# Kernel optimization log

Measured on AMD Instinct MI355X. Metric: run time of the kernel, lower is better.

The kernel has to match this reference:

```python
import jax, jax.numpy as jnp
import numpy as np

BN_EPS = 1e-5

def mish(x):
    return x * jnp.tanh(jax.nn.softplus(x))

def setup_inputs() -> dict:
    key = jax.random.key(0)
    k1, k2, k3 = jax.random.split(key, 3)
    B, C, D, N = 16, 512, 512, 2048
    x = jax.random.normal(k1, (B, C, N), dtype=jnp.float32)
    W = jax.random.normal(k2, (D, C), dtype=jnp.float32) * (1.0 / np.sqrt(C))
    gamma = jnp.ones((D,), dtype=jnp.float32)
    bn_beta = jnp.zeros((D,), dtype=jnp.float32)
    beta = jax.random.normal(k3, (1,), dtype=jnp.float32) * 0.1
    return {"x": x, "W": W, "gamma": gamma, "bn_beta": bn_beta, "beta": beta}

def reference(x, W, gamma, bn_beta, beta):
    # 1x1 conv: [B,C,N] -> [B,D,N]
    q = jnp.einsum('dc,bcn->bdn', W, x)
    # BatchNorm1d (training-mode batch stats, biased variance) over (B, N) per channel
    mean = jnp.mean(q, axis=(0, 2), keepdims=True)
    var = jnp.mean(jnp.square(q - mean), axis=(0, 2), keepdims=True)
    q = (q - mean) * jax.lax.rsqrt(var + BN_EPS)
    q = q * gamma[None, :, None] + bn_beta[None, :, None]
    h = mish(q)                                   # proj_key  [B,D,N]; proj_query = h^T [B,N,D]
    energy = jnp.einsum('bdn,bdm->bnm', h, h)     # bmm(Q, Q^T) -> [B,N,N]
    attn = jax.nn.softmax(energy, axis=-1)
    out_x = jnp.einsum('bdm,bnm->bdn', h, attn)   # bmm(proj_key, attn^T)
    return beta[0] * out_x + h
```

## Files before the change

### kernel.cpp

```cpp
#include <hip/hip_runtime.h>
#include <cstdint>
#include <cstddef>

#define B_DIM 16
#define C_DIM 512
#define D_DIM 512
#define N_DIM 2048
#define NSLOTS 512

typedef _Float16 half8  __attribute__((ext_vector_type(8)));
typedef _Float16 half4v __attribute__((ext_vector_type(4)));
typedef float    floatx4 __attribute__((ext_vector_type(4)));

__device__ __forceinline__ void gload_lds16(const _Float16* g, _Float16* l)
{
    __builtin_amdgcn_global_load_lds((const __attribute__((address_space(1))) void*)g,
                                     (__attribute__((address_space(3))) void*)l,
                                     16, 0, 0);
}

template<int EPI, int TRI, typename OutT>
__global__ __launch_bounds__(256, 4)
void gemm_nt(const _Float16* __restrict__ A, size_t strideA,
             const _Float16* __restrict__ Bm, size_t strideB,
             OutT* __restrict__ Cm, size_t strideC,
             int M, int Ncols, int K,
             const float* __restrict__ beta_ptr,
             const _Float16* __restrict__ Hm, size_t strideH,
             float* __restrict__ st_s, float* __restrict__ st_ss)
{
    constexpr int BK  = 64;
    constexpr int TP  = 136;
    constexpr int SMEM_HALFS = TRI ? (128 * TP) : (128 * 2 * BK);
    __shared__ _Float16 smem[SMEM_HALFS];
    _Float16* sA = smem;
    _Float16* sB = smem + 128 * BK;

    const int gx = gridDim.x, gy = gridDim.y;
    const int nwg = gx * gy * gridDim.z;
    int flat = blockIdx.x + gx * (blockIdx.y + gy * blockIdx.z);
    const int q8 = nwg >> 3;
    flat = (flat & 7) * q8 + (flat >> 3);

    int bx, by, bz;
    if (TRI) {
        int tri = flat % gx;
        bz = flat / gx;
        const int nt = Ncols >> 7;
        int r = 0;
        while (tri >= nt - r) { tri -= nt - r; ++r; }
        bx = r; by = r + tri;
    } else {
        bx = flat % gx;
        by = (flat / gx) % gy;
        bz = flat / (gx * gy);
    }

    const _Float16* Ab = A  + (size_t)bz * strideA;
    const _Float16* Bb = Bm + (size_t)bz * strideB;

    const int m0 = bx * 128;
    const int n0 = by * 128;

    const int tid  = threadIdx.x;
    const int lane = tid & 63;
    const int wv   = tid >> 6;
    const int wr   = (tid >> 7) & 1;
    const int wc   = (tid >> 6) & 1;
    const int fr   = lane & 15;
    const int hi   = lane >> 4;

    const int srow = tid >> 3;
    const int sk   = ((tid & 7) ^ (srow & 7)) * 8;

    const _Float16* gA0 = Ab + (size_t)(m0 + srow) * K + sk;
    const _Float16* gB0 = Bb + (size_t)(n0 + srow) * K + sk;
    _Float16* lA = &sA[(wv * 8) * BK];
    _Float16* lB = &sB[(wv * 8) * BK];

    const int ch0 = ((0 * 4 + hi) ^ (fr & 7)) * 8;
    const int ch1 = ((1 * 4 + hi) ^ (fr & 7)) * 8;
    const _Float16* fA = &sA[(wr * 64 + fr) * BK];
    const _Float16* fB = &sB[(wc * 64 + fr) * BK];

    floatx4 acc[4][4] = {};

    for (int k0 = 0; k0 < K; k0 += BK) {
        __syncthreads();
        #pragma unroll
        for (int p = 0; p < 4; ++p) {
            gload_lds16(gA0 + (size_t)(p * 32) * K + k0, lA + p * 32 * BK);
            gload_lds16(gB0 + (size_t)(p * 32) * K + k0, lB + p * 32 * BK);
        }
        __syncthreads();
        #pragma unroll
        for (int sub = 0; sub < 2; ++sub) {
            const int ch = (sub == 0) ? ch0 : ch1;
            half8 af[4], bf[4];
            #pragma unroll
            for (int i = 0; i < 4; ++i) af[i] = *(const half8*)(fA + i * 16 * BK + ch);
            #pragma unroll
            for (int j = 0; j < 4; ++j) bf[j] = *(const half8*)(fB + j * 16 * BK + ch);
            #pragma unroll
            for (int i = 0; i < 4; ++i)
                #pragma unroll
                for (int j = 0; j < 4; ++j)
                    acc[i][j] = __builtin_amdgcn_mfma_f32_16x16x32_f16(af[i], bf[j], acc[i][j], 0, 0, 0);
        }
    }

    float beta = 0.0f;
    const _Float16* Hb = nullptr;
    if (EPI == 1) { beta = beta_ptr[0]; Hb = Hm + (size_t)bz * strideH; }
    OutT* Cb = Cm + (size_t)bz * strideC;

    const bool mirror = TRI && (bx != by);
    if (mirror) __syncthreads();

    #pragma unroll
    for (int i = 0; i < 4; ++i) {
        const int rowb = m0 + wr * 64 + i * 16 + (hi << 2);
        #pragma unroll
        for (int j = 0; j < 4; ++j) {
            const int col = n0 + wc * 64 + j * 16 + fr;
            half4v mv;
            #pragma unroll
            for (int r = 0; r < 4; ++r) {
                size_t idx = (size_t)(rowb + r) * Ncols + col;
                float v = acc[i][j][r];
                if (EPI == 1) v = beta * v + (float)Hb[idx];
                Cb[idx] = (OutT)v;
                if (TRI) mv[r] = (_Float16)v;
            }
            if (mirror) {
                const int cl = wc * 64 + j * 16 + fr;
                const int rl = wr * 64 + i * 16 + (hi << 2);
                *(half4v*)(smem + cl * TP + rl) = mv;
            }
        }
    }

    if (mirror) {
        __syncthreads();
        #pragma unroll
        for (int k = 0; k < 8; ++k) {
            const int fl = tid + 256 * k;
            const int rr = fl >> 4;
            const int cc = (fl & 15) * 8;
            half8 v = *(const half8*)(smem + rr * TP + cc);
            *(half8*)((_Float16*)(void*)Cb + (size_t)(n0 + rr) * Ncols + m0 + cc) = v;
        }
    }

    if (EPI == 2) {
        const int p = ((bz * gy + by) << 1) + wc;
        #pragma unroll
        for (int i = 0; i < 4; ++i) {
            #pragma unroll
            for (int r = 0; r < 4; ++r) {
                float s = 0.f, ss2 = 0.f;
                #pragma unroll
                for (int j = 0; j < 4; ++j) {
                    float v = acc[i][j][r];
                    s += v; ss2 += v * v;
                }
                #pragma unroll
                for (int o = 1; o < 16; o <<= 1) {
                    s   += __shfl_xor(s,   o, 64);
                    ss2 += __shfl_xor(ss2, o, 64);
                }
                if (fr == 0) {
                    const int d = m0 + wr * 64 + i * 16 + (hi << 2) + r;
                    const size_t slot = (size_t)d * NSLOTS + p;
                    st_s[slot]  = s;
                    st_ss[slot] = ss2;
                }
            }
        }
    }
}

__global__ void transpose_convert_x(const float* __restrict__ x, _Float16* __restrict__ xT,
                                    const float* __restrict__ W, _Float16* __restrict__ Wh)
{
    const int bz = blockIdx.z;
    const int tx = threadIdx.x, ty = threadIdx.y;
    if (bz == B_DIM) {
        const int bid = blockIdx.x + blockIdx.y * gridDim.x;
        const int idx = bid * 256 + ty * 32 + tx;
        if (idx < D_DIM * C_DIM) Wh[idx] = (_Float16)W[idx];
        return;
    }
    __shared__ float tile[32][33];
    const int n0 = blockIdx.x * 32;
    const int c0 = blockIdx.y * 32;
    const float* xb = x + (size_t)bz * C_DIM * N_DIM;
    #pragma unroll
    for (int j = 0; j < 4; ++j)
        tile[ty + j * 8][tx] = xb[(size_t)(c0 + ty + j * 8) * N_DIM + n0 + tx];
    __syncthreads();
    _Float16* xtb = xT + (size_t)bz * N_DIM * C_DIM;
    #pragma unroll
    for (int j = 0; j < 4; ++j)
        xtb[(size_t)(n0 + ty + j * 8) * C_DIM + c0 + tx] = (_Float16)tile[tx][ty + j * 8];
}

__global__ __launch_bounds__(256)
void bn_finalize(const float* __restrict__ st_s, const float* __restrict__ st_ss,
                 const float* __restrict__ gamma, const float* __restrict__ bn_beta,
                 float2* __restrict__ stats)
{
    const int d = blockIdx.x;
    const int tid = threadIdx.x;
    const float* ps = st_s  + (size_t)d * NSLOTS;
    const float* pq = st_ss + (size_t)d * NSLOTS;
    float s  = ps[tid] + ps[tid + 256];
    float ss = pq[tid] + pq[tid + 256];
    #pragma unroll
    for (int o = 32; o; o >>= 1) {
        s  += __shfl_down(s,  o, 64);
        ss += __shfl_down(ss, o, 64);
    }
    __shared__ float red[8];
    const int wv = tid >> 6;
    if ((tid & 63) == 0) { red[wv] = s; red[4 + wv] = ss; }
    __syncthreads();
    if (tid == 0) {
        s  = red[0] + red[1] + red[2] + red[3];
        ss = red[4] + red[5] + red[6] + red[7];
        const float inv = 1.0f / (float)(B_DIM * N_DIM);
        float mean = s * inv;
        float var  = ss * inv - mean * mean;
        float scale = gamma[d] * rsqrtf(var + 1e-5f);
        stats[d] = make_float2(scale, bn_beta[d] - mean * scale);
    }
}

__device__ __forceinline__ float mishf(float v)
{
    float t = __expf(fminf(v, 30.0f));
    float u = 1.0f + t;
    u *= u;
    return v * (u - 1.0f) * __builtin_amdgcn_rcpf(u + 1.0f);
}

__global__ void bn_mish(const _Float16* __restrict__ q, const float2* __restrict__ stats,
                        _Float16* __restrict__ h, _Float16* __restrict__ hT)
{
    __shared__ float tile[32][33];
    const int bz = blockIdx.z;
    const int n0 = blockIdx.x * 32;
    const int d0 = blockIdx.y * 32;
    const int tx = threadIdx.x, ty = threadIdx.y;
    const _Float16* qb = q + (size_t)bz * D_DIM * N_DIM;
    _Float16* hb = h + (size_t)bz * D_DIM * N_DIM;
    #pragma unroll
    for (int j = 0; j < 4; ++j) {
        int d = d0 + ty + j * 8;
        float2 sc = stats[d];
        float v  = (float)qb[(size_t)d * N_DIM + n0 + tx];
        float hv = mishf(v * sc.x + sc.y);
        tile[ty + j * 8][tx] = hv;
        hb[(size_t)d * N_DIM + n0 + tx] = (_Float16)hv;
    }
    __syncthreads();
    _Float16* htb = hT + (size_t)bz * N_DIM * D_DIM;
    #pragma unroll
    for (int j = 0; j < 4; ++j)
        htb[(size_t)(n0 + ty + j * 8) * D_DIM + d0 + tx] = (_Float16)tile[tx][ty + j * 8];
}

__global__ __launch_bounds__(256)
void softmax_rows(const _Float16* __restrict__ energy, size_t strideE,
                  _Float16* __restrict__ attn, size_t strideAt)
{
    const int wid  = threadIdx.x >> 6;
    const int lane = threadIdx.x & 63;
    const int n = blockIdx.x * 4 + wid;
    const int b = blockIdx.y;
    const _Float16* row = energy + (size_t)b * strideE + (size_t)n * N_DIM;
    _Float16*      orow = attn   + (size_t)b * strideAt + (size_t)n * N_DIM;
    float f[32];
    #pragma unroll
    for (int w = 0; w < 4; ++w) {
        half8 v = *(const half8*)(row + w * 512 + lane * 8);
        #pragma unroll
        for (int j = 0; j < 8; ++j) f[w * 8 + j] = (float)v[j];
    }
    float mx = f[0];
    #pragma unroll
    for (int k = 1; k < 32; ++k) mx = fmaxf(mx, f[k]);
    #pragma unroll
    for (int off = 1; off < 64; off <<= 1) mx = fmaxf(mx, __shfl_xor(mx, off, 64));
    float s = 0.f;
    #pragma unroll
    for (int k = 0; k < 32; ++k) { f[k] = __expf(f[k] - mx); s += f[k]; }
    #pragma unroll
    for (int off = 1; off < 64; off <<= 1) s += __shfl_xor(s, off, 64);
    const float inv = 1.0f / s;
    #pragma unroll
    for (int w = 0; w < 4; ++w) {
        half8 o;
        #pragma unroll
        for (int j = 0; j < 8; ++j) o[j] = (_Float16)(f[w * 8 + j] * inv);
        *(half8*)(orow + w * 512 + lane * 8) = o;
    }
}

extern "C" void kernel_launch(void* const* d_in, const int* in_sizes, int n_in,
                              void* d_out, int out_size, void* d_ws, size_t ws_size,
                              hipStream_t stream)
{
    const float* x       = (const float*)d_in[0];
    const float* W       = (const float*)d_in[1];
    const float* gamma   = (const float*)d_in[2];
    const float* bn_beta = (const float*)d_in[3];
    const float* beta    = (const float*)d_in[4];
    float* out = (float*)d_out;

    char* ws = (char*)d_ws;
    size_t off = 0;
    auto take = [&](size_t bytes) -> char* {
        char* p = ws + off;
        off = (off + bytes + 255) & ~(size_t)255;
        return p;
    };

    _Float16* xT    = (_Float16*)take((size_t)B_DIM * N_DIM * C_DIM * 2);
    _Float16* q     = (_Float16*)take((size_t)B_DIM * D_DIM * N_DIM * 2);
    _Float16* h     = (_Float16*)take((size_t)B_DIM * D_DIM * N_DIM * 2);
    _Float16* Wh    = (_Float16*)take((size_t)D_DIM * C_DIM * 2);
    float2*   stats = (float2*)  take((size_t)D_DIM * sizeof(float2));
    float*    st_s  = (float*)   take((size_t)NSLOTS * D_DIM * 4);
    float*    st_ss = (float*)   take((size_t)NSLOTS * D_DIM * 4);
    _Float16* hT    = xT;

    const size_t eSz = (size_t)N_DIM * N_DIM * 2;
    const size_t fixedEnd = off;
    const int full = (ws_size >= fixedEnd + (size_t)B_DIM * eSz + 1024) ? 1 : 0;
    _Float16* energy = (_Float16*)take(full ? (size_t)B_DIM * eSz : eSz);
    _Float16* attn   = energy;

    const int NT = N_DIM / 128;
    const int TRI_BLOCKS = NT * (NT + 1) / 2;

    transpose_convert_x<<<dim3(N_DIM / 32, C_DIM / 32, B_DIM + 1), dim3(32, 8), 0, stream>>>(
        x, xT, W, Wh);
    gemm_nt<2, 0, _Float16><<<dim3(D_DIM / 128, N_DIM / 128, B_DIM), dim3(256), 0, stream>>>(
        Wh, 0, xT, (size_t)N_DIM * C_DIM, q, (size_t)D_DIM * N_DIM,
        D_DIM, N_DIM, C_DIM, nullptr, nullptr, 0, st_s, st_ss);
    bn_finalize<<<dim3(D_DIM), dim3(256), 0, stream>>>(st_s, st_ss, gamma, bn_beta, stats);
    bn_mish<<<dim3(N_DIM / 32, D_DIM / 32, B_DIM), dim3(32, 8), 0, stream>>>(q, stats, h, hT);

    if (full) {
        gemm_nt<0, 1, _Float16><<<dim3(TRI_BLOCKS, 1, B_DIM), dim3(256), 0, stream>>>(
            hT, (size_t)N_DIM * D_DIM, hT, (size_t)N_DIM * D_DIM,
            energy, (size_t)N_DIM * N_DIM, N_DIM, N_DIM, D_DIM,
            nullptr, nullptr, 0, nullptr, nullptr);
        softmax_rows<<<dim3(N_DIM / 4, B_DIM), dim3(256), 0, stream>>>(
            energy, (size_t)N_DIM * N_DIM, attn, (size_t)N_DIM * N_DIM);
        gemm_nt<1, 0, float><<<dim3(D_DIM / 128, N_DIM / 128, B_DIM), dim3(256), 0, stream>>>(
            h, (size_t)D_DIM * N_DIM, attn, (size_t)N_DIM * N_DIM,
            out, (size_t)D_DIM * N_DIM, D_DIM, N_DIM, N_DIM,
            beta, h, (size_t)D_DIM * N_DIM, nullptr, nullptr);
    } else {
        for (int b = 0; b < B_DIM; ++b) {
            const _Float16* hTb = hT + (size_t)b * N_DIM * D_DIM;
            const _Float16* hb  = h  + (size_t)b * D_DIM * N_DIM;
            gemm_nt<0, 1, _Float16><<<dim3(TRI_BLOCKS, 1, 1), dim3(256), 0, stream>>>(
                hTb, 0, hTb, 0, energy, 0, N_DIM, N_DIM, D_DIM,
                nullptr, nullptr, 0, nullptr, nullptr);
            softmax_rows<<<dim3(N_DIM / 4, 1), dim3(256), 0, stream>>>(energy, 0, attn, 0);
            gemm_nt<1, 0, float><<<dim3(D_DIM / 128, N_DIM / 128, 1), dim3(256), 0, stream>>>(
                hb, 0, attn, 0, out + (size_t)b * D_DIM * N_DIM, 0,
                D_DIM, N_DIM, N_DIM, beta, hb, 0, nullptr, nullptr);
        }
    }
}
```

Measured before the change: 229.5 us.

## Add 256x256-tile 8-wave pipelined GEMM for attention-value product

Replaces the 128x128 GEMM used for the h·attn^T product with a dedicated 256x256-tile kernel using 512 threads. Each k-step is split into finely interleaved phases that issue direct global-to-LDS loads for the next tile between MFMA groups, with setprio and explicit waitcnt and barriers. The larger tile raises arithmetic intensity per byte loaded from the large attn matrix. In exchange it uses much more LDS and registers, leaves fewer workgroups (256 per batch set) to fill the CUs, and relies on hand-tuned waitcnt ordering.

Result: slower. 241.5 us (+5.2%).

```diff
diff --git a/kernel.cpp b/kernel.cpp
--- a/kernel.cpp
+++ b/kernel.cpp
@@ -58,7 +58,6 @@
 
     const _Float16* Ab = A  + (size_t)bz * strideA;
     const _Float16* Bb = Bm + (size_t)bz * strideB;
-
     const int m0 = bx * 128;
     const int n0 = by * 128;
 
@@ -180,6 +179,131 @@
     }
 }
 
+#define PHASE8(BUF, MH, KS, STAGES, VM)                                              \
+    {                                                                                 \
+        const _Float16* fA_ = &sA8[BUF][(wr8 * 128 + (MH) * 64 + fr) * BK8];          \
+        const _Float16* fB_ = &sB8[BUF][(wc8 * 64 + fr) * BK8];                       \
+        const int ch_ = (((KS) * 4 + hi) ^ (fr & 7)) * 8;                             \
+        half8 af_[4], bf_[4];                                                         \
+        _Pragma("unroll")                                                             \
+        for (int m_ = 0; m_ < 4; ++m_) af_[m_] = *(const half8*)(fA_ + m_ * 16 * BK8 + ch_); \
+        _Pragma("unroll")                                                             \
+        for (int n_ = 0; n_ < 4; ++n_) bf_[n_] = *(const half8*)(fB_ + n_ * 16 * BK8 + ch_); \
+        __builtin_amdgcn_sched_barrier(0);                                            \
+        STAGES;                                                                       \
+        __builtin_amdgcn_s_barrier();                                                 \
+        asm volatile("s_waitcnt lgkmcnt(0)" ::: "memory");                            \
+        __builtin_amdgcn_s_setprio(1);                                                \
+        _Pragma("unroll")                                                             \
+        for (int m_ = 0; m_ < 4; ++m_)                                                \
+            _Pragma("unroll")                                                         \
+            for (int n_ = 0; n_ < 4; ++n_)                                            \
+                acc[(MH) * 4 + m_][n_] = __builtin_amdgcn_mfma_f32_16x16x32_f16(      \
+                    af_[m_], bf_[n_], acc[(MH) * 4 + m_][n_], 0, 0, 0);               \
+        __builtin_amdgcn_s_setprio(0);                                                \
+        if ((VM) == 0)      asm volatile("s_waitcnt vmcnt(0)" ::: "memory");          \
+        else if ((VM) == 2) asm volatile("s_waitcnt vmcnt(2)" ::: "memory");          \
+        __builtin_amdgcn_s_barrier();                                                 \
+    }
+
+__global__ __launch_bounds__(512)
+void gemm_nt256_pv(const _Float16* __restrict__ A, size_t strideA,
+                   const _Float16* __restrict__ Bm, size_t strideB,
+                   float* __restrict__ Cm, size_t strideC,
+                   int M, int Ncols, int K,
+                   const float* __restrict__ beta_ptr,
+                   const _Float16* __restrict__ Hm, size_t strideH)
+{
+    constexpr int BK8 = 64;
+    __shared__ _Float16 sA8[2][256 * BK8];
+    __shared__ _Float16 sB8[2][256 * BK8];
+
+    const int gx = gridDim.x, gy = gridDim.y;
+    const int nwg = gx * gy * gridDim.z;
+    int flat = blockIdx.x + gx * (blockIdx.y + gy * blockIdx.z);
+    const int q8 = nwg >> 3;
+    flat = (flat & 7) * q8 + (flat >> 3);
+    const int bx = flat % gx;
+    const int by = (flat / gx) % gy;
+    const int bz = flat / (gx * gy);
+
+    const _Float16* Ab = A  + (size_t)bz * strideA;
+    const _Float16* Bb = Bm + (size_t)bz * strideB;
+    const int m0 = bx * 256;
+    const int n0 = by * 256;
+
+    const int tid  = threadIdx.x;
+    const int lane = tid & 63;
+    const int wid  = tid >> 6;
+    const int wr8  = wid >> 2;
+    const int wc8  = wid & 3;
+    const int fr   = lane & 15;
+    const int hi   = lane >> 4;
+
+    const int srow = (wid << 3) + (lane >> 3);
+    const int sk   = ((lane & 7) ^ (srow & 7)) * 8;
+
+    const _Float16* gA = Ab + (size_t)(m0 + srow) * K + sk;
+    const _Float16* gB = Bb + (size_t)(n0 + srow) * K + sk;
+    const int ldsbase = (wid << 3) * BK8;
+
+    auto stageA = [&](int buf, int kt, int half) {
+        const size_t ko = (size_t)kt * BK8;
+        #pragma unroll
+        for (int p = half; p < 4; p += 2)
+            gload_lds16(gA + ko + (size_t)(p * 64) * K, &sA8[buf][ldsbase + p * 64 * BK8]);
+    };
+    auto stageB = [&](int buf, int kt, int half) {
+        const size_t ko = (size_t)kt * BK8;
+        #pragma unroll
+        for (int p = half; p < 4; p += 2)
+            gload_lds16(gB + ko + (size_t)(p * 64) * K, &sB8[buf][ldsbase + p * 64 * BK8]);
+    };
+
+    floatx4 acc[8][4] = {};
+
+    const int nt = K / BK8;
+    const int niter = nt >> 1;
+
+    stageA(0, 0, 0); stageA(0, 0, 1);
+    stageB(0, 0, 0); stageB(0, 0, 1);
+    stageA(1, 1, 0);
+    asm volatile("s_waitcnt vmcnt(2)" ::: "memory");
+    __builtin_amdgcn_s_barrier();
+
+    for (int it = 0; it < niter; ++it) {
+        const int b = 2 * it + 1, c = 2 * it + 2, d = 2 * it + 3;
+        const bool lastc = (c >= nt);
+        const int vm_end = lastc ? 0 : 2;
+        PHASE8(0, 0, 0, { stageA(1, b, 1); stageB(1, b, 0); }, -1)
+        PHASE8(0, 0, 1, { stageB(1, b, 1); }, -1)
+        PHASE8(0, 1, 0, { if (!lastc) stageA(0, c, 0); }, -1)
+        PHASE8(0, 1, 1, {}, vm_end)
+        PHASE8(1, 0, 0, { if (!lastc) { stageA(0, c, 1); stageB(0, c, 0); } }, -1)
+        PHASE8(1, 0, 1, { if (!lastc) stageB(0, c, 1); }, -1)
+        PHASE8(1, 1, 0, { if (!lastc) stageA(1, d, 0); }, -1)
+        PHASE8(1, 1, 1, {}, vm_end)
+    }
+
+    const float beta = beta_ptr[0];
+    const _Float16* Hb = Hm + (size_t)bz * strideH;
+    float* Cb = Cm + (size_t)bz * strideC;
+
+    #pragma unroll
+    for (int i = 0; i < 8; ++i) {
+        const int rowb = m0 + wr8 * 128 + i * 16 + (hi << 2);
+        #pragma unroll
+        for (int j = 0; j < 4; ++j) {
+            const int col = n0 + wc8 * 64 + j * 16 + fr;
+            #pragma unroll
+            for (int r = 0; r < 4; ++r) {
+                size_t idx = (size_t)(rowb + r) * Ncols + col;
+                Cb[idx] = beta * acc[i][j][r] + (float)Hb[idx];
+            }
+        }
+    }
+}
+
 __global__ void transpose_convert_x(const float* __restrict__ x, _Float16* __restrict__ xT,
                                     const float* __restrict__ W, _Float16* __restrict__ Wh)
 {
@@ -359,10 +483,10 @@
             nullptr, nullptr, 0, nullptr, nullptr);
         softmax_rows<<<dim3(N_DIM / 4, B_DIM), dim3(256), 0, stream>>>(
             energy, (size_t)N_DIM * N_DIM, attn, (size_t)N_DIM * N_DIM);
-        gemm_nt<1, 0, float><<<dim3(D_DIM / 128, N_DIM / 128, B_DIM), dim3(256), 0, stream>>>(
+        gemm_nt256_pv<<<dim3(D_DIM / 256, N_DIM / 256, B_DIM), dim3(512), 0, stream>>>(
             h, (size_t)D_DIM * N_DIM, attn, (size_t)N_DIM * N_DIM,
             out, (size_t)D_DIM * N_DIM, D_DIM, N_DIM, N_DIM,
-            beta, h, (size_t)D_DIM * N_DIM, nullptr, nullptr);
+            beta, h, (size_t)D_DIM * N_DIM);
     } else {
         for (int b = 0; b < B_DIM; ++b) {
             const _Float16* hTb = hT + (size_t)b * N_DIM * D_DIM;
@@ -371,9 +495,9 @@
                 hTb, 0, hTb, 0, energy, 0, N_DIM, N_DIM, D_DIM,
                 nullptr, nullptr, 0, nullptr, nullptr);
             softmax_rows<<<dim3(N_DIM / 4, 1), dim3(256), 0, stream>>>(energy, 0, attn, 0);
-            gemm_nt<1, 0, float><<<dim3(D_DIM / 128, N_DIM / 128, 1), dim3(256), 0, stream>>>(
+            gemm_nt256_pv<<<dim3(D_DIM / 256, N_DIM / 256, 1), dim3(512), 0, stream>>>(
                 hb, 0, attn, 0, out + (size_t)b * D_DIM * N_DIM, 0,
-                D_DIM, N_DIM, N_DIM, beta, hb, 0, nullptr, nullptr);
-        }
-    }
-}
+                D_DIM, N_DIM, N_DIM, beta, hb, 0);
+        }
+    }
+}
```
